# Optimization experiments

Hardware: AMD Instinct MI355X
Metric: run time of the kernel (lower is better)

The kernel has to match this reference:

```python
import jax, jax.numpy as jnp
import numpy as np

M, K, N = 4096, 4096, 11008


def setup_inputs() -> dict:
    key = jax.random.key(0)
    k1, k2, k3, k4, k5 = jax.random.split(key, 5)
    x = jax.random.normal(k1, (M, K), dtype=jnp.float32)
    # int8-valued quantized weights stored as int32 for portability
    weight = jax.random.randint(k2, (N, K), -128, 128, dtype=jnp.int32)
    antiquant_scale = jax.random.uniform(k3, (N,), dtype=jnp.float32) * 0.01 + 0.001
    antiquant_offset = jax.random.normal(k4, (N,), dtype=jnp.float32)
    bias = jax.random.normal(k5, (N,), dtype=jnp.float32)
    return {"x": x, "weight": weight, "antiquant_scale": antiquant_scale,
            "antiquant_offset": antiquant_offset, "bias": bias}


def reference(x, weight, antiquant_scale, antiquant_offset, bias):
    # Dequantize per output channel: w_fp[n, k] = (w_int[n, k] + offset[n]) * scale[n]
    w_fp = (weight.astype(x.dtype) + antiquant_offset[:, None]) * antiquant_scale[:, None]
    # y[m, n] = sum_k x[m, k] * w_fp[n, k] + bias[n]
    y = jnp.einsum('mk,nk->mn', x, w_fp) + bias[None, :]
    return y
```

## Files before the change

### kernel.cpp

```cpp
#include <hip/hip_runtime.h>
#include <hip/hip_bf16.h>
#include <cstdint>

#define M_DIM 4096
#define K_DIM 4096
#define N_DIM 11008
#define NT_K  (K_DIM / 64)

typedef __attribute__((ext_vector_type(8))) short short8;
typedef __attribute__((ext_vector_type(4))) float floatx4;

__device__ __forceinline__ unsigned short f2bf(float f) {
    union { float f; unsigned u; } v; v.f = f;
    unsigned r = v.u + 0x7FFFu + ((v.u >> 16) & 1u);
    return (unsigned short)(r >> 16);
}

__device__ __forceinline__ void async_copy16(const ushort* g, const ushort* l) {
    __builtin_amdgcn_global_load_lds(
        (const __attribute__((address_space(1))) void*)(uintptr_t)(const void*)g,
        (__attribute__((address_space(3))) void*)(uintptr_t)(const void*)l,
        16, 0, 0);
}

__global__ void prep_x_kernel(const float* __restrict__ x, ushort* __restrict__ xb,
                              float* __restrict__ s) {
    const int row = blockIdx.x;
    const int tid = threadIdx.x;
    const float*  xr = x  + (size_t)row * K_DIM;
    ushort*       xo = xb + (size_t)row * K_DIM;
    float sum = 0.f;
#pragma unroll
    for (int i = 0; i < 2; ++i) {
        int e = (tid + i * 256) * 8;
        float4 v0 = *(const float4*)(xr + e);
        float4 v1 = *(const float4*)(xr + e + 4);
        sum += v0.x + v0.y + v0.z + v0.w + v1.x + v1.y + v1.z + v1.w;
        short8 o;
        o[0] = f2bf(v0.x); o[1] = f2bf(v0.y); o[2] = f2bf(v0.z); o[3] = f2bf(v0.w);
        o[4] = f2bf(v1.x); o[5] = f2bf(v1.y); o[6] = f2bf(v1.z); o[7] = f2bf(v1.w);
        *(short8*)(xo + e) = o;
    }
#pragma unroll
    for (int off = 32; off > 0; off >>= 1) sum += __shfl_down(sum, off, 64);
    __shared__ float red[4];
    if ((tid & 63) == 0) red[tid >> 6] = sum;
    __syncthreads();
    if (tid == 0) s[row] = red[0] + red[1] + red[2] + red[3];
}

__global__ void prep_w_kernel(const int* __restrict__ w, ushort* __restrict__ wb) {
    size_t i = (size_t)blockIdx.x * blockDim.x + threadIdx.x;
    const int4* wi = (const int4*)w;
    int4 v0 = wi[2 * i];
    int4 v1 = wi[2 * i + 1];
    short8 o;
    o[0] = f2bf((float)v0.x); o[1] = f2bf((float)v0.y);
    o[2] = f2bf((float)v0.z); o[3] = f2bf((float)v0.w);
    o[4] = f2bf((float)v1.x); o[5] = f2bf((float)v1.y);
    o[6] = f2bf((float)v1.z); o[7] = f2bf((float)v1.w);
    ((short8*)wb)[i] = o;
}


#define BAR_MID()                               \
    __builtin_amdgcn_sched_barrier(0);          \
    __builtin_amdgcn_s_barrier();               \
    asm volatile("s_waitcnt lgkmcnt(0)");       \
    __builtin_amdgcn_sched_barrier(0)

#define BAR_END()                               \
    __builtin_amdgcn_sched_barrier(0);          \
    __builtin_amdgcn_s_barrier()

#define LOAD_A(q)                                                             \
    _Pragma("unroll")                                                         \
    for (int fl = 0; fl < 2; ++fl)                                            \
        _Pragma("unroll")                                                     \
        for (int ks = 0; ks < 2; ++ks)                                        \
            a[fl][ks] = *(const short8*)(Ar + aoff[ks] + (q) * 2048 + fl * 1024)

#define MFMA_Q(q)                                                             \
    __builtin_amdgcn_s_setprio(1);                                            \
    _Pragma("unroll")                                                         \
    for (int fl = 0; fl < 2; ++fl)                                            \
        _Pragma("unroll")                                                     \
        for (int fn = 0; fn < 4; ++fn)                                        \
            _Pragma("unroll")                                                 \
            for (int ks = 0; ks < 2; ++ks)                                    \
                acc[(q) * 2 + fl][fn] = __builtin_amdgcn_mfma_f32_16x16x32_bf16( \
                    a[fl][ks], b[fn][ks], acc[(q) * 2 + fl][fn], 0, 0, 0);    \
    __builtin_amdgcn_s_setprio(0)

__global__ __launch_bounds__(512) void gemm_kernel(
        const ushort* __restrict__ xb, const ushort* __restrict__ wb,
        const float* __restrict__ s, const float* __restrict__ scale,
        const float* __restrict__ offset, const float* __restrict__ bias,
        float* __restrict__ y) {
    __shared__ ushort lds[2][2][256 * 64];

    const int tid  = threadIdx.x;
    const int lane = tid & 63;
    const int wave = tid >> 6;
    const int wm   = wave >> 2;
    const int wn   = wave & 3;
    const int r15  = lane & 15;
    const int quad = lane >> 4;

    const int wg  = blockIdx.x;
    const int swz = (wg & 7) * 86 + (wg >> 3);
    const int m0  = (swz & 15) * 256;
    const int n0  = (swz >> 4) * 256;

    const int    srow = wave * 8 + (lane >> 3);
    const int    scol = ((lane & 7) ^ (lane >> 3)) * 8;
    const ushort* aSrc = xb + (size_t)(m0 + srow) * K_DIM + scol;
    const ushort* bSrc = wb + (size_t)(n0 + srow) * K_DIM + scol;
    const int    sdst = wave * 512;

    const int x7 = r15 & 7;
    int aoff[2], boff[2];
#pragma unroll
    for (int ks = 0; ks < 2; ++ks) {
        aoff[ks] = (wm * 128 + r15) * 64 + ((ks * 4 + quad) ^ x7) * 8;
        boff[ks] = (wn *  64 + r15) * 64 + ((ks * 4 + quad) ^ x7) * 8;
    }

    floatx4 acc[8][4] = {};

#pragma unroll
    for (int l = 0; l < 4; ++l)
        async_copy16(aSrc + (size_t)l * 64 * K_DIM, &lds[0][0][sdst + l * 4096]);
#pragma unroll
    for (int l = 0; l < 4; ++l)
        async_copy16(bSrc + (size_t)l * 64 * K_DIM, &lds[0][1][sdst + l * 4096]);
#pragma unroll
    for (int l = 0; l < 4; ++l)
        async_copy16(bSrc + (size_t)l * 64 * K_DIM + 64, &lds[1][1][sdst + l * 4096]);
    asm volatile("s_waitcnt vmcnt(4)" ::: "memory");
    __builtin_amdgcn_s_barrier();

    for (int t = 0; t < NT_K; ++t) {
        const int c = t & 1;
        const ushort* Ar = &lds[c][0][0];
        ushort*       Aw = &lds[c ^ 1][0][0];
        ushort*       Bp = &lds[c][1][0];
        const size_t ka = (t + 1 < NT_K) ? (size_t)(t + 1) * 64 : 0;
        const size_t kb = (t + 2 < NT_K) ? (size_t)(t + 2) * 64 : 0;
        short8 a[2][2], b[4][2];

#pragma unroll
        for (int fn = 0; fn < 4; ++fn)
#pragma unroll
            for (int ks = 0; ks < 2; ++ks)
                b[fn][ks] = *(const short8*)(Bp + boff[ks] + fn * 1024);
        LOAD_A(0);
        async_copy16(aSrc + ka,                        Aw + sdst);
        async_copy16(aSrc + (size_t) 64 * K_DIM + ka,  Aw + sdst + 4096);
        BAR_MID();
        MFMA_Q(0);
        BAR_END();

        LOAD_A(1);
        async_copy16(aSrc + (size_t)128 * K_DIM + ka,  Aw + sdst + 8192);
        async_copy16(aSrc + (size_t)192 * K_DIM + ka,  Aw + sdst + 12288);
        BAR_MID();
        MFMA_Q(1);
        BAR_END();

        LOAD_A(2);
        async_copy16(bSrc + kb,                        Bp + sdst);
        async_copy16(bSrc + (size_t) 64 * K_DIM + kb,  Bp + sdst + 4096);
        BAR_MID();
        MFMA_Q(2);
        BAR_END();

        LOAD_A(3);
        async_copy16(bSrc + (size_t)128 * K_DIM + kb,  Bp + sdst + 8192);
        async_copy16(bSrc + (size_t)192 * K_DIM + kb,  Bp + sdst + 12288);
        BAR_MID();
        MFMA_Q(3);
        asm volatile("s_waitcnt vmcnt(4)" ::: "memory");
        BAR_END();
    }

    float sm[8][4];
#pragma unroll
    for (int fm = 0; fm < 8; ++fm)
#pragma unroll
        for (int r = 0; r < 4; ++r)
            sm[fm][r] = s[m0 + wm * 128 + fm * 16 + quad * 4 + r];

#pragma unroll
    for (int fn = 0; fn < 4; ++fn) {
        const int n = n0 + wn * 64 + fn * 16 + r15;
        const float sc = scale[n], of = offset[n], bi = bias[n];
#pragma unroll
        for (int fm = 0; fm < 8; ++fm) {
            const int mb = m0 + wm * 128 + fm * 16 + quad * 4;
#pragma unroll
            for (int r = 0; r < 4; ++r) {
                y[(size_t)(mb + r) * N_DIM + n] =
                    sc * (acc[fm][fn][r] + of * sm[fm][r]) + bi;
            }
        }
    }
}

extern "C" void kernel_launch(void* const* d_in, const int* in_sizes, int n_in,
                              void* d_out, int out_size, void* d_ws, size_t ws_size,
                              hipStream_t stream) {
    const float* x      = (const float*)d_in[0];
    const int*   weight = (const int*)d_in[1];
    const float* scale  = (const float*)d_in[2];
    const float* offset = (const float*)d_in[3];
    const float* bias   = (const float*)d_in[4];
    float*       y      = (float*)d_out;

    ushort* xb = (ushort*)d_ws;
    ushort* wb = (ushort*)((char*)d_ws + (size_t)M_DIM * K_DIM * 2);
    float*  s  = (float*)((char*)d_ws + (size_t)M_DIM * K_DIM * 2 + (size_t)N_DIM * K_DIM * 2);

    prep_x_kernel<<<M_DIM, 256, 0, stream>>>(x, xb, s);
    int wblocks = (int)(((size_t)N_DIM * K_DIM / 8) / 256);
    prep_w_kernel<<<wblocks, 256, 0, stream>>>(weight, wb);

    gemm_kernel<<<dim3((N_DIM / 256) * (M_DIM / 256)), dim3(512), 0, stream>>>(
        xb, wb, s, scale, offset, bias, y);
}
```

Baseline: 670.5 us.

## Software-pipeline LDS fragment loads with double registers and fuse prep kernels

The GEMM main loop is unrolled by two and uses double-buffered register fragments (a0/a1, b0/b1). The next A quarter and the next tile's B fragments are read from LDS while the current MFMA quarter runs, and the explicit lgkmcnt(0) wait before each MFMA block is removed. The two preprocessing kernels (x to bf16 with row sums, weight to bf16) are merged into one launch, with each weight block now handling 4096 elements. The goal is to hide LDS read latency behind matrix math and save one kernel launch. The cost is higher VGPR pressure, and the barrier ordering for LDS buffer reuse now depends on compiler-inserted waits.

```diff
diff --git a/kernel.cpp b/kernel.cpp
--- a/kernel.cpp
+++ b/kernel.cpp
@@ -23,64 +23,71 @@
         16, 0, 0);
 }
 
-__global__ void prep_x_kernel(const float* __restrict__ x, ushort* __restrict__ xb,
-                              float* __restrict__ s) {
-    const int row = blockIdx.x;
+__global__ void prep_kernel(const float* __restrict__ x, const int* __restrict__ w,
+                            ushort* __restrict__ xb, ushort* __restrict__ wb,
+                            float* __restrict__ s) {
     const int tid = threadIdx.x;
-    const float*  xr = x  + (size_t)row * K_DIM;
-    ushort*       xo = xb + (size_t)row * K_DIM;
-    float sum = 0.f;
-#pragma unroll
-    for (int i = 0; i < 2; ++i) {
-        int e = (tid + i * 256) * 8;
-        float4 v0 = *(const float4*)(xr + e);
-        float4 v1 = *(const float4*)(xr + e + 4);
-        sum += v0.x + v0.y + v0.z + v0.w + v1.x + v1.y + v1.z + v1.w;
-        short8 o;
-        o[0] = f2bf(v0.x); o[1] = f2bf(v0.y); o[2] = f2bf(v0.z); o[3] = f2bf(v0.w);
-        o[4] = f2bf(v1.x); o[5] = f2bf(v1.y); o[6] = f2bf(v1.z); o[7] = f2bf(v1.w);
-        *(short8*)(xo + e) = o;
-    }
-#pragma unroll
-    for (int off = 32; off > 0; off >>= 1) sum += __shfl_down(sum, off, 64);
-    __shared__ float red[4];
-    if ((tid & 63) == 0) red[tid >> 6] = sum;
-    __syncthreads();
-    if (tid == 0) s[row] = red[0] + red[1] + red[2] + red[3];
-}
-
-__global__ void prep_w_kernel(const int* __restrict__ w, ushort* __restrict__ wb) {
-    size_t i = (size_t)blockIdx.x * blockDim.x + threadIdx.x;
-    const int4* wi = (const int4*)w;
-    int4 v0 = wi[2 * i];
-    int4 v1 = wi[2 * i + 1];
-    short8 o;
-    o[0] = f2bf((float)v0.x); o[1] = f2bf((float)v0.y);
-    o[2] = f2bf((float)v0.z); o[3] = f2bf((float)v0.w);
-    o[4] = f2bf((float)v1.x); o[5] = f2bf((float)v1.y);
-    o[6] = f2bf((float)v1.z); o[7] = f2bf((float)v1.w);
-    ((short8*)wb)[i] = o;
-}
-
-
-#define BAR_MID()                               \
+    if (blockIdx.x < M_DIM) {
+        const int row = blockIdx.x;
+        const float*  xr = x  + (size_t)row * K_DIM;
+        ushort*       xo = xb + (size_t)row * K_DIM;
+        float sum = 0.f;
+#pragma unroll
+        for (int i = 0; i < 2; ++i) {
+            int e = (tid + i * 256) * 8;
+            float4 v0 = *(const float4*)(xr + e);
+            float4 v1 = *(const float4*)(xr + e + 4);
+            sum += v0.x + v0.y + v0.z + v0.w + v1.x + v1.y + v1.z + v1.w;
+            short8 o;
+            o[0] = f2bf(v0.x); o[1] = f2bf(v0.y); o[2] = f2bf(v0.z); o[3] = f2bf(v0.w);
+            o[4] = f2bf(v1.x); o[5] = f2bf(v1.y); o[6] = f2bf(v1.z); o[7] = f2bf(v1.w);
+            *(short8*)(xo + e) = o;
+        }
+#pragma unroll
+        for (int off = 32; off > 0; off >>= 1) sum += __shfl_down(sum, off, 64);
+        __shared__ float red[4];
+        if ((tid & 63) == 0) red[tid >> 6] = sum;
+        __syncthreads();
+        if (tid == 0) s[row] = red[0] + red[1] + red[2] + red[3];
+    } else {
+        const size_t base = (size_t)(blockIdx.x - M_DIM) * 4096;
+        const int4* wi = (const int4*)w + (base >> 2) + tid * 4;
+        short8*     wo = (short8*)wb + (base >> 3) + tid * 2;
+#pragma unroll
+        for (int h = 0; h < 2; ++h) {
+            int4 v0 = wi[h * 2];
+            int4 v1 = wi[h * 2 + 1];
+            short8 o;
+            o[0] = f2bf((float)v0.x); o[1] = f2bf((float)v0.y);
+            o[2] = f2bf((float)v0.z); o[3] = f2bf((float)v0.w);
+            o[4] = f2bf((float)v1.x); o[5] = f2bf((float)v1.y);
+            o[6] = f2bf((float)v1.z); o[7] = f2bf((float)v1.w);
+            wo[h] = o;
+        }
+    }
+}
+
+
+#define BAR()                                   \
     __builtin_amdgcn_sched_barrier(0);          \
     __builtin_amdgcn_s_barrier();               \
-    asm volatile("s_waitcnt lgkmcnt(0)");       \
     __builtin_amdgcn_sched_barrier(0)
 
-#define BAR_END()                               \
-    __builtin_amdgcn_sched_barrier(0);          \
-    __builtin_amdgcn_s_barrier()
-
-#define LOAD_A(q)                                                             \
+#define LDA(dst, base, q)                                                     \
     _Pragma("unroll")                                                         \
     for (int fl = 0; fl < 2; ++fl)                                            \
         _Pragma("unroll")                                                     \
         for (int ks = 0; ks < 2; ++ks)                                        \
-            a[fl][ks] = *(const short8*)(Ar + aoff[ks] + (q) * 2048 + fl * 1024)
-
-#define MFMA_Q(q)                                                             \
+            dst[fl][ks] = *(const short8*)((const ushort*)(base) + aoff[ks] + (q) * 2048 + fl * 1024)
+
+#define LDB(dst, base)                                                        \
+    _Pragma("unroll")                                                         \
+    for (int fn = 0; fn < 4; ++fn)                                            \
+        _Pragma("unroll")                                                     \
+        for (int ks = 0; ks < 2; ++ks)                                        \
+            dst[fn][ks] = *(const short8*)((const ushort*)(base) + boff[ks] + fn * 1024)
+
+#define MFMAQ(ar, bc, q)                                                      \
     __builtin_amdgcn_s_setprio(1);                                            \
     _Pragma("unroll")                                                         \
     for (int fl = 0; fl < 2; ++fl)                                            \
@@ -89,8 +96,36 @@
             _Pragma("unroll")                                                 \
             for (int ks = 0; ks < 2; ++ks)                                    \
                 acc[(q) * 2 + fl][fn] = __builtin_amdgcn_mfma_f32_16x16x32_bf16( \
-                    a[fl][ks], b[fn][ks], acc[(q) * 2 + fl][fn], 0, 0, 0);    \
+                    ar[fl][ks], bc[fn][ks], acc[(q) * 2 + fl][fn], 0, 0, 0);  \
     __builtin_amdgcn_s_setprio(0)
+
+#define TILE(KA, KB, AR, AW, BW, BRN, BC, BN)                                 \
+                                                                     \
+    BAR();                                                                    \
+    async_copy16(aSrc + (KA),                      (AW) + sdst);              \
+    async_copy16(aSrc + (size_t) 64 * K_DIM + (KA), (AW) + sdst + 4096);      \
+    LDA(a1, AR, 1);                                                           \
+    MFMAQ(a0, BC, 0);                                                         \
+                                                                     \
+    BAR();                                                                    \
+    async_copy16(aSrc + (size_t)128 * K_DIM + (KA), (AW) + sdst + 8192);      \
+    async_copy16(aSrc + (size_t)192 * K_DIM + (KA), (AW) + sdst + 12288);     \
+    LDA(a0, AR, 2);                                                           \
+    MFMAQ(a1, BC, 1);                                                         \
+                                                                     \
+    BAR();                                                                    \
+    async_copy16(bSrc + (KB),                      (BW) + sdst);              \
+    async_copy16(bSrc + (size_t) 64 * K_DIM + (KB), (BW) + sdst + 4096);      \
+    LDA(a1, AR, 3);                                                           \
+    MFMAQ(a0, BC, 2);                                                         \
+     \
+    async_copy16(bSrc + (size_t)128 * K_DIM + (KB), (BW) + sdst + 8192);      \
+    async_copy16(bSrc + (size_t)192 * K_DIM + (KB), (BW) + sdst + 12288);     \
+    asm volatile("s_waitcnt vmcnt(4)" ::: "memory");                          \
+    BAR();                                                                    \
+    LDB(BN, BRN);                                                             \
+    LDA(a0, AW, 0);                                                           \
+    MFMAQ(a1, BC, 3)
 
 __global__ __launch_bounds__(512) void gemm_kernel(
         const ushort* __restrict__ xb, const ushort* __restrict__ wb,
@@ -126,62 +161,35 @@
         boff[ks] = (wn *  64 + r15) * 64 + ((ks * 4 + quad) ^ x7) * 8;
     }
 
+    ushort* lds0A = &lds[0][0][0];
+    ushort* lds1A = &lds[1][0][0];
+    ushort* lds0B = &lds[0][1][0];
+    ushort* lds1B = &lds[1][1][0];
+
     floatx4 acc[8][4] = {};
+    short8 a0[2][2], a1[2][2], b0[4][2], b1[4][2];
 
 #pragma unroll
     for (int l = 0; l < 4; ++l)
-        async_copy16(aSrc + (size_t)l * 64 * K_DIM, &lds[0][0][sdst + l * 4096]);
+        async_copy16(aSrc + (size_t)l * 64 * K_DIM, lds0A + sdst + l * 4096);
 #pragma unroll
     for (int l = 0; l < 4; ++l)
-        async_copy16(bSrc + (size_t)l * 64 * K_DIM, &lds[0][1][sdst + l * 4096]);
+        async_copy16(bSrc + (size_t)l * 64 * K_DIM, lds0B + sdst + l * 4096);
 #pragma unroll
     for (int l = 0; l < 4; ++l)
-        async_copy16(bSrc + (size_t)l * 64 * K_DIM + 64, &lds[1][1][sdst + l * 4096]);
+        async_copy16(bSrc + (size_t)l * 64 * K_DIM + 64, lds1B + sdst + l * 4096);
     asm volatile("s_waitcnt vmcnt(4)" ::: "memory");
     __builtin_amdgcn_s_barrier();
-
-    for (int t = 0; t < NT_K; ++t) {
-        const int c = t & 1;
-        const ushort* Ar = &lds[c][0][0];
-        ushort*       Aw = &lds[c ^ 1][0][0];
-        ushort*       Bp = &lds[c][1][0];
-        const size_t ka = (t + 1 < NT_K) ? (size_t)(t + 1) * 64 : 0;
-        const size_t kb = (t + 2 < NT_K) ? (size_t)(t + 2) * 64 : 0;
-        short8 a[2][2], b[4][2];
-
-#pragma unroll
-        for (int fn = 0; fn < 4; ++fn)
-#pragma unroll
-            for (int ks = 0; ks < 2; ++ks)
-                b[fn][ks] = *(const short8*)(Bp + boff[ks] + fn * 1024);
-        LOAD_A(0);
-        async_copy16(aSrc + ka,                        Aw + sdst);
-        async_copy16(aSrc + (size_t) 64 * K_DIM + ka,  Aw + sdst + 4096);
-        BAR_MID();
-        MFMA_Q(0);
-        BAR_END();
-
-        LOAD_A(1);
-        async_copy16(aSrc + (size_t)128 * K_DIM + ka,  Aw + sdst + 8192);
-        async_copy16(aSrc + (size_t)192 * K_DIM + ka,  Aw + sdst + 12288);
-        BAR_MID();
-        MFMA_Q(1);
-        BAR_END();
-
-        LOAD_A(2);
-        async_copy16(bSrc + kb,                        Bp + sdst);
-        async_copy16(bSrc + (size_t) 64 * K_DIM + kb,  Bp + sdst + 4096);
-        BAR_MID();
-        MFMA_Q(2);
-        BAR_END();
-
-        LOAD_A(3);
-        async_copy16(bSrc + (size_t)128 * K_DIM + kb,  Bp + sdst + 8192);
-        async_copy16(bSrc + (size_t)192 * K_DIM + kb,  Bp + sdst + 12288);
-        BAR_MID();
-        MFMA_Q(3);
-        asm volatile("s_waitcnt vmcnt(4)" ::: "memory");
-        BAR_END();
+    LDB(b0, lds0B);
+    LDA(a0, lds0A, 0);
+
+    for (int t = 0; t < NT_K; t += 2) {
+        const size_t ka0 = (size_t)(t + 1) * 64;
+        const size_t kb0 = (t + 2 < NT_K) ? (size_t)(t + 2) * 64 : 0;
+        TILE(ka0, kb0, lds0A, lds1A, lds0B, lds1B, b0, b1);
+        const size_t ka1 = (t + 2 < NT_K) ? (size_t)(t + 2) * 64 : 0;
+        const size_t kb1 = (t + 3 < NT_K) ? (size_t)(t + 3) * 64 : 0;
+        TILE(ka1, kb1, lds1A, lds0A, lds1B, lds0B, b1, b0);
     }
 
     float sm[8][4];
@@ -221,9 +229,8 @@
     ushort* wb = (ushort*)((char*)d_ws + (size_t)M_DIM * K_DIM * 2);
     float*  s  = (float*)((char*)d_ws + (size_t)M_DIM * K_DIM * 2 + (size_t)N_DIM * K_DIM * 2);
 
-    prep_x_kernel<<<M_DIM, 256, 0, stream>>>(x, xb, s);
-    int wblocks = (int)(((size_t)N_DIM * K_DIM / 8) / 256);
-    prep_w_kernel<<<wblocks, 256, 0, stream>>>(weight, wb);
+    prep_kernel<<<M_DIM + (int)((size_t)N_DIM * K_DIM / 4096), 256, 0, stream>>>(
+        x, weight, xb, wb, s);
 
     gemm_kernel<<<dim3((N_DIM / 256) * (M_DIM / 256)), dim3(512), 0, stream>>>(
         xb, wb, s, scale, offset, bias, y);
```

Result: no change. 664.4 us (-0.9%).
